# Optimization experiments

Measured on AMD Instinct MI355X. Metric: run time of the kernel, lower is better.

Reference implementation:

```python
import jax, jax.numpy as jnp
import numpy as np

NFRAMES = 8
N_ITERS = 32        # fixed-iteration Riemannian gradient descent (geomstats FrechetMean equivalent)
EPS = 1e-7


def _l2norm(x, axis=-1):
    return x / jnp.maximum(jnp.linalg.norm(x, axis=axis, keepdims=True), EPS)


def _frechet_mean_sphere(X):
    """Batched Frechet mean on the unit hypersphere.
    X: [..., n, d] unit vectors. Returns [..., d] unit mean.
    Iteration: mu <- Exp_mu( mean_i Log_mu(x_i) ).
    """
    mu0 = _l2norm(jnp.mean(X, axis=-2))

    def step(mu, _):
        dots = jnp.clip(jnp.einsum('...d,...kd->...k', mu, X), -1.0 + 1e-6, 1.0 - 1e-6)
        theta = jnp.arccos(dots)
        safe = theta > 1e-4
        coef = jnp.where(safe, theta / jnp.sin(jnp.where(safe, theta, 1.0)), 1.0)
        # Log map: [..., n, d]
        logs = coef[..., None] * (X - dots[..., None] * mu[..., None, :])
        v = jnp.mean(logs, axis=-2)                      # tangent mean [..., d]
        vn = jnp.linalg.norm(v, axis=-1, keepdims=True)
        vsafe = vn > 1e-9
        sinc = jnp.where(vsafe, jnp.sin(vn) / jnp.where(vsafe, vn, 1.0), 1.0)
        mu_new = jnp.cos(vn) * mu + sinc * v             # Exp map
        return _l2norm(mu_new), None

    mu, _ = jax.lax.scan(step, mu0, None, length=N_ITERS)
    return mu


def setup_inputs() -> dict:
    key = jax.random.key(0)
    k1, k2 = jax.random.split(key)
    support_vecs = jax.random.normal(k1, (25, 64, NFRAMES * 2048), dtype=jnp.float32)
    target_vec = jax.random.normal(k2, (64, NFRAMES * 2048), dtype=jnp.float32)
    return {"support_vecs": support_vecs, "target_vec": target_vec}


def reference(support_vecs, target_vec):
    seqlen, bs, df = support_vecs.shape
    sup = _l2norm(support_vecs.reshape(seqlen, bs, NFRAMES, -1))   # [s,b,n,2048]
    tgt = _l2norm(target_vec.reshape(bs, NFRAMES, -1))             # [b,n,2048]
    support_means = _frechet_mean_sphere(sup)                      # [s,b,2048]
    target_means = _frechet_mean_sphere(tgt)                       # [b,2048]
    similarities = jnp.einsum('sbd,bd->sb', support_means, target_means)
    return similarities
```

## Files before the change

kernel.cpp:

```cpp
#include <hip/hip_runtime.h>
#include <math.h>

#define NFR 8
#define DD 2048
#define NS 25
#define NB 64
#define NPAIR (NS*NB)
#define NITER 32
#define TILE 256
#define NT (DD/TILE)
#define RSTRIDE 260
#define BUFSZ (16*RSTRIDE)

typedef __attribute__((ext_vector_type(8))) short short8;
typedef __attribute__((ext_vector_type(4))) float f32x4;

__device__ __forceinline__ float acos_fast(float x) {
    const float ax = fabsf(x);
    const bool big = ax > 0.5f;
    const float z = big ? 0.5f * (1.f - ax) : x * x;
    const float s = big ? sqrtf(z) : ax;
    float p = fmaf(z, 4.2163199048e-2f, 2.4181311049e-2f);
    p = fmaf(z, p, 4.5470025998e-2f);
    p = fmaf(z, p, 7.4953002686e-2f);
    p = fmaf(z, p, 1.6666752422e-1f);
    const float asin_s = fmaf(s * z, p, s);
    const float asin_abs = big ? (1.5707963267948966f - 2.f * asin_s) : asin_s;
    return 1.5707963267948966f - copysignf(asin_abs, x);
}

#define SPLIT2(a, b, HI, LO) { \
    const float ha_ = __uint_as_float(__float_as_uint(a) & 0xFFFF0000u); \
    const float hb_ = __uint_as_float(__float_as_uint(b) & 0xFFFF0000u); \
    HI = __builtin_amdgcn_perm(__float_as_uint(b), __float_as_uint(a), 0x07060302u); \
    LO = __builtin_amdgcn_perm(__float_as_uint((b) - hb_), __float_as_uint((a) - ha_), 0x07060302u); \
}

__device__ __forceinline__ void load_lds16(const float* g, float* l) {
    __builtin_amdgcn_global_load_lds(
        (const __attribute__((address_space(1))) void*)g,
        (__attribute__((address_space(3))) void*)l, 16, 0, 0);
}

__global__ __launch_bounds__(256) void fused_kernel(const float* __restrict__ sup,
                                                    const float* __restrict__ tgt,
                                                    float* __restrict__ out) {
    const int p   = blockIdx.x;
    const int b   = p & (NB - 1);
    const int tid = threadIdx.x;
    const int wv  = tid >> 6;
    const int l   = tid & 63;
    const int row = l & 15;
    const int kg  = l >> 4;

    __shared__ float lds[2 * BUFSZ];
    float* part = lds;
    float* graw = lds + 2176;

    const float* srow[4];
    #pragma unroll
    for (int i = 0; i < 4; ++i) {
        const int r = wv + 4 * i;
        srow[i] = (r < 8) ? sup + ((size_t)p * NFR + r) * DD + l * 4
                          : tgt + ((size_t)b * NFR + (r - 8)) * DD + l * 4;
    }

    f32x4 accA = {0.f, 0.f, 0.f, 0.f};
    f32x4 accB = {0.f, 0.f, 0.f, 0.f};

    #pragma unroll
    for (int i = 0; i < 4; ++i)
        load_lds16(srow[i], lds + (wv + 4 * i) * RSTRIDE);
    __syncthreads();

    #pragma unroll
    for (int t = 0; t < NT; ++t) {
        if (t + 1 < NT) {
            float* dbuf = lds + ((t + 1) & 1) * BUFSZ;
            #pragma unroll
            for (int i = 0; i < 4; ++i)
                load_lds16(srow[i] + (t + 1) * TILE, dbuf + (wv + 4 * i) * RSTRIDE);
        }
        const float* fb = lds + (t & 1) * BUFSZ + row * RSTRIDE + wv * 64 + kg * 8;
        #pragma unroll
        for (int c2 = 0; c2 < 2; ++c2) {
            const float4 f0 = *(const float4*)(fb + c2 * 32);
            const float4 f1 = *(const float4*)(fb + c2 * 32 + 4);
            union { unsigned int u[4]; short8 s8; } H, L;
            SPLIT2(f0.x, f0.y, H.u[0], L.u[0]);
            SPLIT2(f0.z, f0.w, H.u[1], L.u[1]);
            SPLIT2(f1.x, f1.y, H.u[2], L.u[2]);
            SPLIT2(f1.z, f1.w, H.u[3], L.u[3]);
            accA = __builtin_amdgcn_mfma_f32_16x16x32_bf16(H.s8, H.s8, accA, 0, 0, 0);
            accB = __builtin_amdgcn_mfma_f32_16x16x32_bf16(H.s8, L.s8, accB, 0, 0, 0);
            accB = __builtin_amdgcn_mfma_f32_16x16x32_bf16(L.s8, H.s8, accB, 0, 0, 0);
        }
        __syncthreads();
    }

    #pragma unroll
    for (int r = 0; r < 4; ++r)
        part[wv * 272 + (kg * 4 + r) * 17 + row] = accA[r] + accB[r];
    __syncthreads();

    {
        const int rr = tid >> 4, cc = tid & 15;
        float s = part[rr * 17 + cc] + part[272 + rr * 17 + cc]
                + part[544 + rr * 17 + cc] + part[816 + rr * 17 + cc];
        __syncthreads();
        graw[rr * 16 + cc] = s;
    }
    __syncthreads();

    if (tid < 16) {
        const int j = tid & 7;
        const int base = tid & 8;
        const int R = base + j;
        const int cb = base;

        const float invn_own = rsqrtf(fmaxf(graw[R * 16 + R], 1e-14f));
        float Grow[8];
        #pragma unroll
        for (int k = 0; k < 8; ++k) {
            const float invk = rsqrtf(fmaxf(graw[(cb + k) * 16 + (cb + k)], 1e-14f));
            Grow[k] = graw[R * 16 + cb + k] * invn_own * invk;
        }

        float rs = 0.f;
        #pragma unroll
        for (int k = 0; k < 8; ++k) rs += Grow[k];
        rs += __shfl_xor(rs, 1, 8);
        rs += __shfl_xor(rs, 2, 8);
        rs += __shfl_xor(rs, 4, 8);
        float a_own = rsqrtf(fmaxf(rs, 6.4e-13f));
        float aAll[8];
        #pragma unroll
        for (int k = 0; k < 8; ++k) aAll[k] = a_own;

        for (int it = 0; it < NITER; ++it) {
            float dot = 0.f;
            #pragma unroll
            for (int k = 0; k < 8; ++k) dot = fmaf(Grow[k], aAll[k], dot);
            dot = fminf(fmaxf(dot, -1.f + 1e-6f), 1.f - 1e-6f);
            const float theta = acos_fast(dot);
            const float q = fmaf(-dot, dot, 1.0f);
            const float coef = (theta > 1e-4f) ? theta * rsqrtf(q) : 1.f;
            const float w = 0.125f * coef;
            float wAll[8];
            #pragma unroll
            for (int k = 0; k < 8; ++k) wAll[k] = __shfl(w, base + k, 16);
            float Gw = 0.f;
            #pragma unroll
            for (int k = 0; k < 8; ++k) Gw = fmaf(Grow[k], wAll[k], Gw);
            float u1 = a_own * Gw, u2 = w * Gw;
            u1 += __shfl_xor(u1, 1, 8);  u2 += __shfl_xor(u2, 1, 8);
            u1 += __shfl_xor(u1, 2, 8);  u2 += __shfl_xor(u2, 2, 8);
            u1 += __shfl_xor(u1, 4, 8);  u2 += __shfl_xor(u2, 4, 8);
            const float cdavg = u1;
            const float vnsq = fmaxf(u2 - cdavg * cdavg, 0.f);
            const float vn = sqrtf(vnsq);
            const float rev = vn * 0.15915494309189535f;
            const float sinv = __builtin_amdgcn_sinf(rev);
            const float cosv = __builtin_amdgcn_cosf(rev);
            const float sinc = (vn > 1e-9f) ? sinv / vn : 1.f;
            const float cn2 = fmaf(sinc * sinc, vnsq, cosv * cosv);
            const float rn = rsqrtf(fmaxf(cn2, 1e-14f));
            a_own = (cosv * a_own + sinc * fmaf(-cdavg, a_own, w)) * rn;
            #pragma unroll
            for (int k = 0; k < 8; ++k)
                aAll[k] = (cosv * aAll[k] + sinc * fmaf(-cdavg, aAll[k], wAll[k])) * rn;
        }

        const float ahat = a_own * invn_own;
        float at[8];
        #pragma unroll
        for (int q2 = 0; q2 < 8; ++q2) at[q2] = __shfl(ahat, 8 + q2, 16);
        float tacc = 0.f;
        #pragma unroll
        for (int q2 = 0; q2 < 8; ++q2) tacc = fmaf(graw[j * 16 + 8 + q2], at[q2], tacc);
        float sim = ahat * tacc;
        sim += __shfl_xor(sim, 1, 8);
        sim += __shfl_xor(sim, 2, 8);
        sim += __shfl_xor(sim, 4, 8);
        if (tid == 0) out[p] = sim;
    }
}

extern "C" void kernel_launch(void* const* d_in, const int* in_sizes, int n_in,
                              void* d_out, int out_size, void* d_ws, size_t ws_size,
                              hipStream_t stream) {
    const float* sup = (const float*)d_in[0];
    const float* tgt = (const float*)d_in[1];
    float* out = (float*)d_out;
    fused_kernel<<<NPAIR, 256, 0, stream>>>(sup, tgt, out);
}
```

Measured before the change: 61.83 us.

## Split Gram computation across K-halves and batch the Frechet solve in a second kernel

Replaces the single fused kernel with two. The first is a Gram kernel of 3200 blocks of 512 threads; each block loads half the feature dimension in one shot into swizzled LDS and writes packed triangular Gram partials to workspace. The second is a solve kernel that sums the partials and runs the 32-iteration Frechet mean for 16 pairs per block, so the serial tail no longer runs on only 16 threads of a large block. This adds more parallelism and XCD-aware block ordering. The cost is a second launch, a workspace round trip, and target Gram blocks computed redundantly but written only once.

Measured after the change: 53.10 us. 1.16x faster.

```diff
diff --git a/kernel.cpp b/kernel.cpp
--- a/kernel.cpp
+++ b/kernel.cpp
@@ -7,10 +7,8 @@
 #define NB 64
 #define NPAIR (NS*NB)
 #define NITER 32
-#define TILE 256
-#define NT (DD/TILE)
-#define RSTRIDE 260
-#define BUFSZ (16*RSTRIDE)
+#define WS_TGT 320000
+#define SOLVE_BLKS 100
 
 typedef __attribute__((ext_vector_type(8))) short short8;
 typedef __attribute__((ext_vector_type(4))) float f32x4;
@@ -42,148 +40,188 @@
         (__attribute__((address_space(3))) void*)l, 16, 0, 0);
 }
 
-__global__ __launch_bounds__(256) void fused_kernel(const float* __restrict__ sup,
-                                                    const float* __restrict__ tgt,
-                                                    float* __restrict__ out) {
-    const int p   = blockIdx.x;
-    const int b   = p & (NB - 1);
+__global__ __launch_bounds__(512) void gram_kernel(const float* __restrict__ sup,
+                                                   const float* __restrict__ tgt,
+                                                   float* __restrict__ ws) {
+    const int bid = blockIdx.x;
+    const int xcd = bid & 7;
+    const int q   = bid >> 3;
+    const int b   = xcd * 8 + (q & 7);
+    const int sq  = q >> 3;
+    const int s   = sq % NS;
+    const int kh  = sq / NS;
+    const int p   = s * NB + b;
     const int tid = threadIdx.x;
     const int wv  = tid >> 6;
     const int l   = tid & 63;
     const int row = l & 15;
     const int kg  = l >> 4;
 
-    __shared__ float lds[2 * BUFSZ];
-    float* part = lds;
-    float* graw = lds + 2176;
-
-    const float* srow[4];
-    #pragma unroll
-    for (int i = 0; i < 4; ++i) {
-        const int r = wv + 4 * i;
-        srow[i] = (r < 8) ? sup + ((size_t)p * NFR + r) * DD + l * 4
-                          : tgt + ((size_t)b * NFR + (r - 8)) * DD + l * 4;
-    }
+    __shared__ float lds[16384];
+
+    #pragma unroll
+    for (int i = 0; i < 2; ++i) {
+        const int r  = 2 * wv + i;
+        const int r7 = r & 7;
+        const float* g = (r < 8)
+            ? sup + ((size_t)p * NFR + r) * DD + kh * 1024
+            : tgt + ((size_t)b * NFR + (r - 8)) * DD + kh * 1024;
+        const float* gl = g + (size_t)((l ^ r7) * 4);
+        float* d = lds + r * 1024;
+        #pragma unroll
+        for (int c = 0; c < 4; ++c)
+            load_lds16(gl + c * 256, d + c * 256);
+    }
+    __syncthreads();
 
     f32x4 accA = {0.f, 0.f, 0.f, 0.f};
     f32x4 accB = {0.f, 0.f, 0.f, 0.f};
-
-    #pragma unroll
-    for (int i = 0; i < 4; ++i)
-        load_lds16(srow[i], lds + (wv + 4 * i) * RSTRIDE);
-    __syncthreads();
-
-    #pragma unroll
-    for (int t = 0; t < NT; ++t) {
-        if (t + 1 < NT) {
-            float* dbuf = lds + ((t + 1) & 1) * BUFSZ;
-            #pragma unroll
-            for (int i = 0; i < 4; ++i)
-                load_lds16(srow[i] + (t + 1) * TILE, dbuf + (wv + 4 * i) * RSTRIDE);
-        }
-        const float* fb = lds + (t & 1) * BUFSZ + row * RSTRIDE + wv * 64 + kg * 8;
-        #pragma unroll
-        for (int c2 = 0; c2 < 2; ++c2) {
-            const float4 f0 = *(const float4*)(fb + c2 * 32);
-            const float4 f1 = *(const float4*)(fb + c2 * 32 + 4);
-            union { unsigned int u[4]; short8 s8; } H, L;
-            SPLIT2(f0.x, f0.y, H.u[0], L.u[0]);
-            SPLIT2(f0.z, f0.w, H.u[1], L.u[1]);
-            SPLIT2(f1.x, f1.y, H.u[2], L.u[2]);
-            SPLIT2(f1.z, f1.w, H.u[3], L.u[3]);
-            accA = __builtin_amdgcn_mfma_f32_16x16x32_bf16(H.s8, H.s8, accA, 0, 0, 0);
-            accB = __builtin_amdgcn_mfma_f32_16x16x32_bf16(H.s8, L.s8, accB, 0, 0, 0);
-            accB = __builtin_amdgcn_mfma_f32_16x16x32_bf16(L.s8, H.s8, accB, 0, 0, 0);
-        }
-        __syncthreads();
-    }
-
+    const int swz = (row & 7) << 4;
+    const char* rowbase = (const char*)lds + row * 4096;
+    #pragma unroll
+    for (int st = 0; st < 4; ++st) {
+        const int o0 = (wv * 128 + st * 32) * 4 + kg * 32;
+        const float4 f0 = *(const float4*)(rowbase + (o0 ^ swz));
+        const float4 f1 = *(const float4*)(rowbase + ((o0 + 16) ^ swz));
+        union { unsigned int u[4]; short8 s8; } H, L;
+        SPLIT2(f0.x, f0.y, H.u[0], L.u[0]);
+        SPLIT2(f0.z, f0.w, H.u[1], L.u[1]);
+        SPLIT2(f1.x, f1.y, H.u[2], L.u[2]);
+        SPLIT2(f1.z, f1.w, H.u[3], L.u[3]);
+        accA = __builtin_amdgcn_mfma_f32_16x16x32_bf16(H.s8, H.s8, accA, 0, 0, 0);
+        accB = __builtin_amdgcn_mfma_f32_16x16x32_bf16(H.s8, L.s8, accB, 0, 0, 0);
+        accB = __builtin_amdgcn_mfma_f32_16x16x32_bf16(L.s8, H.s8, accB, 0, 0, 0);
+    }
+    __syncthreads();
+
+    float* part = lds;
     #pragma unroll
     for (int r = 0; r < 4; ++r)
         part[wv * 272 + (kg * 4 + r) * 17 + row] = accA[r] + accB[r];
     __syncthreads();
 
-    {
+    if (tid < 256) {
         const int rr = tid >> 4, cc = tid & 15;
-        float s = part[rr * 17 + cc] + part[272 + rr * 17 + cc]
-                + part[544 + rr * 17 + cc] + part[816 + rr * 17 + cc];
-        __syncthreads();
-        graw[rr * 16 + cc] = s;
-    }
-    __syncthreads();
-
-    if (tid < 16) {
-        const int j = tid & 7;
-        const int base = tid & 8;
-        const int R = base + j;
-        const int cb = base;
-
-        const float invn_own = rsqrtf(fmaxf(graw[R * 16 + R], 1e-14f));
-        float Grow[8];
-        #pragma unroll
-        for (int k = 0; k < 8; ++k) {
-            const float invk = rsqrtf(fmaxf(graw[(cb + k) * 16 + (cb + k)], 1e-14f));
-            Grow[k] = graw[R * 16 + cb + k] * invn_own * invk;
+        float v = 0.f;
+        #pragma unroll
+        for (int w = 0; w < 8; ++w) v += part[w * 272 + rr * 17 + cc];
+        if (rr < 8) {
+            if (cc >= 8)
+                ws[(size_t)(p * 2 + kh) * 100 + 36 + rr * 8 + (cc - 8)] = v;
+            else if (cc >= rr)
+                ws[(size_t)(p * 2 + kh) * 100 + rr * 8 + cc - rr * (rr + 1) / 2] = v;
+        } else if (s == 0 && cc >= rr) {
+            const int i8 = rr - 8, j8 = cc - 8;
+            ws[WS_TGT + (size_t)(b * 2 + kh) * 36 + i8 * 8 + j8 - i8 * (i8 + 1) / 2] = v;
         }
-
-        float rs = 0.f;
-        #pragma unroll
-        for (int k = 0; k < 8; ++k) rs += Grow[k];
-        rs += __shfl_xor(rs, 1, 8);
-        rs += __shfl_xor(rs, 2, 8);
-        rs += __shfl_xor(rs, 4, 8);
-        float a_own = rsqrtf(fmaxf(rs, 6.4e-13f));
-        float aAll[8];
-        #pragma unroll
-        for (int k = 0; k < 8; ++k) aAll[k] = a_own;
-
-        for (int it = 0; it < NITER; ++it) {
-            float dot = 0.f;
-            #pragma unroll
-            for (int k = 0; k < 8; ++k) dot = fmaf(Grow[k], aAll[k], dot);
-            dot = fminf(fmaxf(dot, -1.f + 1e-6f), 1.f - 1e-6f);
-            const float theta = acos_fast(dot);
-            const float q = fmaf(-dot, dot, 1.0f);
-            const float coef = (theta > 1e-4f) ? theta * rsqrtf(q) : 1.f;
-            const float w = 0.125f * coef;
-            float wAll[8];
-            #pragma unroll
-            for (int k = 0; k < 8; ++k) wAll[k] = __shfl(w, base + k, 16);
-            float Gw = 0.f;
-            #pragma unroll
-            for (int k = 0; k < 8; ++k) Gw = fmaf(Grow[k], wAll[k], Gw);
-            float u1 = a_own * Gw, u2 = w * Gw;
-            u1 += __shfl_xor(u1, 1, 8);  u2 += __shfl_xor(u2, 1, 8);
-            u1 += __shfl_xor(u1, 2, 8);  u2 += __shfl_xor(u2, 2, 8);
-            u1 += __shfl_xor(u1, 4, 8);  u2 += __shfl_xor(u2, 4, 8);
-            const float cdavg = u1;
-            const float vnsq = fmaxf(u2 - cdavg * cdavg, 0.f);
-            const float vn = sqrtf(vnsq);
-            const float rev = vn * 0.15915494309189535f;
-            const float sinv = __builtin_amdgcn_sinf(rev);
-            const float cosv = __builtin_amdgcn_cosf(rev);
-            const float sinc = (vn > 1e-9f) ? sinv / vn : 1.f;
-            const float cn2 = fmaf(sinc * sinc, vnsq, cosv * cosv);
-            const float rn = rsqrtf(fmaxf(cn2, 1e-14f));
-            a_own = (cosv * a_own + sinc * fmaf(-cdavg, a_own, w)) * rn;
-            #pragma unroll
-            for (int k = 0; k < 8; ++k)
-                aAll[k] = (cosv * aAll[k] + sinc * fmaf(-cdavg, aAll[k], wAll[k])) * rn;
+    }
+}
+
+__global__ __launch_bounds__(256) void solve_kernel(const float* __restrict__ ws,
+                                                    float* __restrict__ out) {
+    const int bid = blockIdx.x;
+    const int tid = threadIdx.x;
+    __shared__ float synth[16 * 256];
+
+    for (int e = tid; e < 4096; e += 256) {
+        const int pp = e >> 8, ij = e & 255;
+        const int i = ij >> 4, j = ij & 15;
+        const int p = bid * 16 + pp;
+        const int b = p & (NB - 1);
+        float v = 0.f;
+        if (i < 8) {
+            if (j < 8) {
+                const int ii = i < j ? i : j, jj = i < j ? j : i;
+                const int t36 = ii*8 + jj - ii*(ii+1)/2;
+                v = ws[(size_t)(p*2+0)*100 + t36] + ws[(size_t)(p*2+1)*100 + t36];
+            } else {
+                const int c64 = 36 + i*8 + (j-8);
+                v = ws[(size_t)(p*2+0)*100 + c64] + ws[(size_t)(p*2+1)*100 + c64];
+            }
+        } else if (j >= 8) {
+            const int i8 = i - 8, j8 = j - 8;
+            const int ii = i8 < j8 ? i8 : j8, jj = i8 < j8 ? j8 : i8;
+            const int t36 = ii*8 + jj - ii*(ii+1)/2;
+            v = ws[WS_TGT + (size_t)(b*2+0)*36 + t36] + ws[WS_TGT + (size_t)(b*2+1)*36 + t36];
         }
-
-        const float ahat = a_own * invn_own;
-        float at[8];
-        #pragma unroll
-        for (int q2 = 0; q2 < 8; ++q2) at[q2] = __shfl(ahat, 8 + q2, 16);
-        float tacc = 0.f;
-        #pragma unroll
-        for (int q2 = 0; q2 < 8; ++q2) tacc = fmaf(graw[j * 16 + 8 + q2], at[q2], tacc);
-        float sim = ahat * tacc;
-        sim += __shfl_xor(sim, 1, 8);
-        sim += __shfl_xor(sim, 2, 8);
-        sim += __shfl_xor(sim, 4, 8);
-        if (tid == 0) out[p] = sim;
-    }
+        synth[e] = v;
+    }
+    __syncthreads();
+
+    const int pp = tid >> 4;
+    const int t16 = tid & 15;
+    const int p = bid * 16 + pp;
+    const float* graw = synth + pp * 256;
+    const int j = t16 & 7;
+    const int base = t16 & 8;
+    const int R = base + j;
+    const int cb = base;
+
+    const float invn_own = rsqrtf(fmaxf(graw[R * 16 + R], 1e-14f));
+    float Grow[8];
+    #pragma unroll
+    for (int k = 0; k < 8; ++k) {
+        const float invk = rsqrtf(fmaxf(graw[(cb + k) * 16 + (cb + k)], 1e-14f));
+        Grow[k] = graw[R * 16 + cb + k] * invn_own * invk;
+    }
+
+    float rs = 0.f;
+    #pragma unroll
+    for (int k = 0; k < 8; ++k) rs += Grow[k];
+    rs += __shfl_xor(rs, 1, 8);
+    rs += __shfl_xor(rs, 2, 8);
+    rs += __shfl_xor(rs, 4, 8);
+    float a_own = rsqrtf(fmaxf(rs, 6.4e-13f));
+    float aAll[8];
+    #pragma unroll
+    for (int k = 0; k < 8; ++k) aAll[k] = a_own;
+
+    for (int it = 0; it < NITER; ++it) {
+        float dot = 0.f;
+        #pragma unroll
+        for (int k = 0; k < 8; ++k) dot = fmaf(Grow[k], aAll[k], dot);
+        dot = fminf(fmaxf(dot, -1.f + 1e-6f), 1.f - 1e-6f);
+        const float theta = acos_fast(dot);
+        const float q = fmaf(-dot, dot, 1.0f);
+        const float coef = (theta > 1e-4f) ? theta * rsqrtf(q) : 1.f;
+        const float w = 0.125f * coef;
+        float wAll[8];
+        #pragma unroll
+        for (int k = 0; k < 8; ++k) wAll[k] = __shfl(w, base + k, 16);
+        float Gw = 0.f;
+        #pragma unroll
+        for (int k = 0; k < 8; ++k) Gw = fmaf(Grow[k], wAll[k], Gw);
+        float u1 = a_own * Gw, u2 = w * Gw;
+        u1 += __shfl_xor(u1, 1, 8);  u2 += __shfl_xor(u2, 1, 8);
+        u1 += __shfl_xor(u1, 2, 8);  u2 += __shfl_xor(u2, 2, 8);
+        u1 += __shfl_xor(u1, 4, 8);  u2 += __shfl_xor(u2, 4, 8);
+        const float cdavg = u1;
+        const float vnsq = fmaxf(u2 - cdavg * cdavg, 0.f);
+        const float vn = sqrtf(vnsq);
+        const float rev = vn * 0.15915494309189535f;
+        const float sinv = __builtin_amdgcn_sinf(rev);
+        const float cosv = __builtin_amdgcn_cosf(rev);
+        const float sinc = (vn > 1e-9f) ? sinv / vn : 1.f;
+        const float cn2 = fmaf(sinc * sinc, vnsq, cosv * cosv);
+        const float rn = rsqrtf(fmaxf(cn2, 1e-14f));
+        a_own = (cosv * a_own + sinc * fmaf(-cdavg, a_own, w)) * rn;
+        #pragma unroll
+        for (int k = 0; k < 8; ++k)
+            aAll[k] = (cosv * aAll[k] + sinc * fmaf(-cdavg, aAll[k], wAll[k])) * rn;
+    }
+
+    const float ahat = a_own * invn_own;
+    float at[8];
+    #pragma unroll
+    for (int q2 = 0; q2 < 8; ++q2) at[q2] = __shfl(ahat, 8 + q2, 16);
+    float tacc = 0.f;
+    #pragma unroll
+    for (int q2 = 0; q2 < 8; ++q2) tacc = fmaf(graw[j * 16 + 8 + q2], at[q2], tacc);
+    float sim = ahat * tacc;
+    sim += __shfl_xor(sim, 1, 8);
+    sim += __shfl_xor(sim, 2, 8);
+    sim += __shfl_xor(sim, 4, 8);
+    if (t16 == 0) out[p] = sim;
 }
 
 extern "C" void kernel_launch(void* const* d_in, const int* in_sizes, int n_in,
@@ -191,6 +229,8 @@
                               hipStream_t stream) {
     const float* sup = (const float*)d_in[0];
     const float* tgt = (const float*)d_in[1];
+    float* ws = (float*)d_ws;
     float* out = (float*)d_out;
-    fused_kernel<<<NPAIR, 256, 0, stream>>>(sup, tgt, out);
-}
+    gram_kernel<<<NPAIR * 2, 512, 0, stream>>>(sup, tgt, ws);
+    solve_kernel<<<SOLVE_BLKS, 256, 0, stream>>>(ws, out);
+}
```
